# Optimization experiments

Hardware: AMD Instinct MI355X
Metric: run time of the kernel (lower is better)

Reference implementation:

```python
import jax, jax.numpy as jnp
import numpy as np

NUM_NODES = 1_000_000
EMBED_DIM = 128
BATCH = 65536
NEG_K = 5


def setup_inputs() -> dict:
    key = jax.random.key(0)
    k1, k2, k3, k4 = jax.random.split(key, 4)
    init_range = 0.5 / EMBED_DIM
    u_weight = jax.random.uniform(k1, (NUM_NODES, EMBED_DIM), jnp.float32,
                                  minval=-init_range, maxval=init_range)
    # v_embeddings initialized to zero in the original; use small random values
    # instead so gradients/scores are non-degenerate for testing.
    v_weight = jax.random.uniform(k2, (NUM_NODES, EMBED_DIM), jnp.float32,
                                  minval=-init_range, maxval=init_range)
    center_nodes = jax.random.randint(k3, (BATCH,), 0, NUM_NODES, jnp.int64 if jax.config.jax_enable_x64 else jnp.int32)
    k5, k6 = jax.random.split(k4)
    context_nodes = jax.random.randint(k5, (BATCH,), 0, NUM_NODES, center_nodes.dtype)
    negative_nodes = jax.random.randint(k6, (BATCH, NEG_K), 0, NUM_NODES, center_nodes.dtype)
    return {
        "center_nodes": center_nodes,
        "context_nodes": context_nodes,
        "negative_nodes": negative_nodes,
        "u_weight": u_weight,
        "v_weight": v_weight,
    }


def reference(center_nodes, context_nodes, negative_nodes, u_weight, v_weight):
    emb_center = u_weight[center_nodes]        # [B, D]
    emb_context = v_weight[context_nodes]      # [B, D]
    emb_negative = v_weight[negative_nodes]    # [B, K, D]

    pos_score = jnp.sum(emb_center * emb_context, axis=1)          # [B]
    pos_loss = jax.nn.log_sigmoid(pos_score)                       # [B]

    neg_score = jnp.einsum('bkd,bd->bk', emb_negative, emb_center)  # [B, K]
    neg_loss = jax.nn.log_sigmoid(-neg_score).sum(axis=1)          # [B]

    return -(pos_loss + neg_loss).mean()
```

## Files before the change

kernel.cpp:

```cpp
#include <hip/hip_runtime.h>
#include <math.h>

#define BATCH 65536
#define DIM 128
#define NEG_K 5

__device__ __forceinline__ float wave_reduce_sum(float v) {
    #pragma unroll
    for (int off = 32; off > 0; off >>= 1)
        v += __shfl_xor(v, off, 64);
    return v;
}

__device__ __forceinline__ float log_sigmoid(float x) {
    return fminf(x, 0.0f) - log1pf(__expf(-fabsf(x)));
}

__global__ void sg_zero(float* ws) {
    if (threadIdx.x == 0 && blockIdx.x == 0) ws[0] = 0.0f;
}

__global__ __launch_bounds__(256) void sg_loss(
    const int* __restrict__ center, const int* __restrict__ context,
    const int* __restrict__ negs, const float* __restrict__ u_w,
    const float* __restrict__ v_w, float* __restrict__ ws)
{
    const int lane = threadIdx.x & 63;
    const int wib  = threadIdx.x >> 6;
    const int wave_id   = blockIdx.x * (blockDim.x >> 6) + wib;
    const int num_waves = gridDim.x * (blockDim.x >> 6);

    float local = 0.0f;
    for (int b = wave_id; b < BATCH; b += num_waves) {
        const size_t c_row = (size_t)center[b]  * DIM;
        const size_t t_row = (size_t)context[b] * DIM;
        const float2 c = ((const float2*)(u_w + c_row))[lane];
        const float2 t = ((const float2*)(v_w + t_row))[lane];

        float pp = c.x * t.x + c.y * t.y;
        float pn[NEG_K];
        #pragma unroll
        for (int k = 0; k < NEG_K; ++k) {
            const size_t n_row = (size_t)negs[b * NEG_K + k] * DIM;
            const float2 nv = ((const float2*)(v_w + n_row))[lane];
            pn[k] = c.x * nv.x + c.y * nv.y;
        }

        float acc = log_sigmoid(wave_reduce_sum(pp));
        #pragma unroll
        for (int k = 0; k < NEG_K; ++k)
            acc += log_sigmoid(-wave_reduce_sum(pn[k]));

        local -= acc;
    }

    __shared__ float sdata[4];
    if (lane == 0) sdata[wib] = local;
    __syncthreads();
    if (threadIdx.x == 0) {
        float s = sdata[0] + sdata[1] + sdata[2] + sdata[3];
        atomicAdd(ws, s);
    }
}

__global__ void sg_finalize(const float* ws, float* out) {
    if (threadIdx.x == 0 && blockIdx.x == 0)
        out[0] = ws[0] / (float)BATCH;
}

extern "C" void kernel_launch(void* const* d_in, const int* in_sizes, int n_in,
                              void* d_out, int out_size, void* d_ws, size_t ws_size,
                              hipStream_t stream) {
    const int*   center  = (const int*)  d_in[0];
    const int*   context = (const int*)  d_in[1];
    const int*   negs    = (const int*)  d_in[2];
    const float* u_w     = (const float*)d_in[3];
    const float* v_w     = (const float*)d_in[4];
    float* out = (float*)d_out;
    float* ws  = (float*)d_ws;

    sg_zero<<<1, 64, 0, stream>>>(ws);
    sg_loss<<<2048, 256, 0, stream>>>(center, context, negs, u_w, v_w, ws);
    sg_finalize<<<1, 64, 0, stream>>>(ws, out);
}
```

Before: 802.8 us.

## Process two samples per wave with half-wave float4 gathers and fuse finalize

Splits each 64-lane wave into two 32-lane halves that each handle one sample, using float4 loads and 5-step shuffle reductions. The loop trip count is fixed and unrolled by 2 to raise memory-level parallelism on the random row gathers. The finalize kernel is removed by scaling inside the atomic add directly to the output. This adds register pressure, and the loop bound is now hardcoded to the grid size.

```diff
diff --git a/kernel.cpp b/kernel.cpp
--- a/kernel.cpp
+++ b/kernel.cpp
@@ -4,8 +4,17 @@
 #define BATCH 65536
 #define DIM 128
 #define NEG_K 5
+#define NWAVES 8192
+#define PAIRS  (BATCH / 2)
 
-__device__ __forceinline__ float wave_reduce_sum(float v) {
+__device__ __forceinline__ float half_reduce(float v) {
+    #pragma unroll
+    for (int off = 16; off > 0; off >>= 1)
+        v += __shfl_xor(v, off, 64);
+    return v;
+}
+
+__device__ __forceinline__ float full_reduce(float v) {
     #pragma unroll
     for (int off = 32; off > 0; off >>= 1)
         v += __shfl_xor(v, off, 64);
@@ -16,56 +25,58 @@
     return fminf(x, 0.0f) - log1pf(__expf(-fabsf(x)));
 }
 
-__global__ void sg_zero(float* ws) {
-    if (threadIdx.x == 0 && blockIdx.x == 0) ws[0] = 0.0f;
+__global__ void sg_zero(float* out) {
+    if (threadIdx.x == 0 && blockIdx.x == 0) out[0] = 0.0f;
 }
 
 __global__ __launch_bounds__(256) void sg_loss(
     const int* __restrict__ center, const int* __restrict__ context,
     const int* __restrict__ negs, const float* __restrict__ u_w,
-    const float* __restrict__ v_w, float* __restrict__ ws)
+    const float* __restrict__ v_w, float* __restrict__ out)
 {
-    const int lane = threadIdx.x & 63;
-    const int wib  = threadIdx.x >> 6;
-    const int wave_id   = blockIdx.x * (blockDim.x >> 6) + wib;
-    const int num_waves = gridDim.x * (blockDim.x >> 6);
+    const int tid  = threadIdx.x;
+    const int lane = tid & 63;
+    const int half = lane >> 5;
+    const int sl   = lane & 31;
+    const int wib  = tid >> 6;
+    const int wave_id = blockIdx.x * (blockDim.x >> 6) + wib;
 
     float local = 0.0f;
-    for (int b = wave_id; b < BATCH; b += num_waves) {
+    #pragma unroll 2
+    for (int it = 0; it < PAIRS / NWAVES; ++it) {
+        const int b = 2 * (wave_id + it * NWAVES) + half;
+
         const size_t c_row = (size_t)center[b]  * DIM;
         const size_t t_row = (size_t)context[b] * DIM;
-        const float2 c = ((const float2*)(u_w + c_row))[lane];
-        const float2 t = ((const float2*)(v_w + t_row))[lane];
+        const float4 c = ((const float4*)(u_w + c_row))[sl];
+        const float4 t = ((const float4*)(v_w + t_row))[sl];
 
-        float pp = c.x * t.x + c.y * t.y;
+        float pp = c.x * t.x + c.y * t.y + c.z * t.z + c.w * t.w;
         float pn[NEG_K];
         #pragma unroll
         for (int k = 0; k < NEG_K; ++k) {
             const size_t n_row = (size_t)negs[b * NEG_K + k] * DIM;
-            const float2 nv = ((const float2*)(v_w + n_row))[lane];
-            pn[k] = c.x * nv.x + c.y * nv.y;
+            const float4 nv = ((const float4*)(v_w + n_row))[sl];
+            pn[k] = c.x * nv.x + c.y * nv.y + c.z * nv.z + c.w * nv.w;
         }
 
-        float acc = log_sigmoid(wave_reduce_sum(pp));
+        float acc = log_sigmoid(half_reduce(pp));
         #pragma unroll
         for (int k = 0; k < NEG_K; ++k)
-            acc += log_sigmoid(-wave_reduce_sum(pn[k]));
+            acc += log_sigmoid(-half_reduce(pn[k]));
 
         local -= acc;
     }
 
+    float wsum = full_reduce(local * (1.0f / 32.0f));
+
     __shared__ float sdata[4];
-    if (lane == 0) sdata[wib] = local;
+    if (lane == 0) sdata[wib] = wsum;
     __syncthreads();
-    if (threadIdx.x == 0) {
+    if (tid == 0) {
         float s = sdata[0] + sdata[1] + sdata[2] + sdata[3];
-        atomicAdd(ws, s);
+        atomicAdd(out, s * (1.0f / (float)BATCH));
     }
-}
-
-__global__ void sg_finalize(const float* ws, float* out) {
-    if (threadIdx.x == 0 && blockIdx.x == 0)
-        out[0] = ws[0] / (float)BATCH;
 }
 
 extern "C" void kernel_launch(void* const* d_in, const int* in_sizes, int n_in,
@@ -77,9 +88,7 @@
     const float* u_w     = (const float*)d_in[3];
     const float* v_w     = (const float*)d_in[4];
     float* out = (float*)d_out;
-    float* ws  = (float*)d_ws;
 
-    sg_zero<<<1, 64, 0, stream>>>(ws);
-    sg_loss<<<2048, 256, 0, stream>>>(center, context, negs, u_w, v_w, ws);
-    sg_finalize<<<1, 64, 0, stream>>>(ws, out);
+    sg_zero<<<1, 64, 0, stream>>>(out);
+    sg_loss<<<2048, 256, 0, stream>>>(center, context, negs, u_w, v_w, out);
 }
```

Measured after the change: 796.9 us. Within noise of the previous version (-0.7%).
